# Performance work log

Hardware: AMD Instinct MI355X
Metric: run time of the kernel (lower is better)

The kernel has to match this reference:

```python
import jax, jax.numpy as jnp
import numpy as np

N, D = 8192, 128

def _rbf_kernel(x, y):
    # InfoVAE-style kernel: exp(-mean((x_i - y_j)^2) / dim) = exp(-sqdist / dim^2)
    dim = x.shape[1]
    x2 = jnp.sum(x * x, axis=1)              # [n]
    y2 = jnp.sum(y * y, axis=1)              # [m]
    sqdist = x2[:, None] + y2[None, :] - 2.0 * (x @ y.T)  # [n, m]
    return jnp.exp(-sqdist / (dim * dim))


def setup_inputs() -> dict:
    key = jax.random.key(0)
    k1, k2 = jax.random.split(key)
    inputs = jax.random.normal(k1, (N, D), dtype=jnp.float32)
    true_samples = jax.random.normal(k2, (N, D), dtype=jnp.float32)
    return {"inputs": inputs, "true_samples": true_samples}


def reference(inputs, true_samples):
    x = true_samples  # samples from standard normal prior
    y = inputs
    k_xx = _rbf_kernel(x, x)
    k_yy = _rbf_kernel(y, y)
    k_xy = _rbf_kernel(x, y)
    mmd = jnp.mean(k_xx) + jnp.mean(k_yy) - 2.0 * jnp.mean(k_xy)
    return mmd
```

## Files before the change

kernel.cpp:

```cpp
#include <hip/hip_runtime.h>
#include <hip/hip_bf16.h>
#include <math.h>


#define NN 8192
#define DD 128
#define TZ 16384
#define SPLIT 12
#define NBLK (64 * SPLIT)

typedef __attribute__((ext_vector_type(8))) short bf16x8;
typedef __attribute__((ext_vector_type(4))) float f32x4;
typedef __attribute__((ext_vector_type(2))) float f32x2;

#if __has_builtin(__builtin_amdgcn_exp2f)
#define EXP2F __builtin_amdgcn_exp2f
#else
#define EXP2F exp2f
#endif

constexpr float LOG2E = 0x1.715476p+0f;
constexpr float S2 = LOG2E / 8192.0f;

constexpr size_t PLANE = 1048576;

#define LDS_RED 32768

constexpr size_t WS_NORM = 2048;
constexpr size_t WS_Z    = WS_NORM + (size_t)TZ * sizeof(float);

__device__ __forceinline__ void gload_lds16(const void* g, void* l) {
  __builtin_amdgcn_global_load_lds(
      (const __attribute__((address_space(1))) void*)g,
      (__attribute__((address_space(3))) void*)l, 16, 0, 0);
}

__global__ __launch_bounds__(256) void prep(
    const float* __restrict__ X, const float* __restrict__ Y,
    char* __restrict__ Zs, float* __restrict__ normZ,
    double* __restrict__ sums) {
  if (blockIdx.x == 0) sums[threadIdx.x] = 0.0;

  const int row = blockIdx.x * 4 + (threadIdx.x >> 6);
  const int lane = threadIdx.x & 63;
  const float* __restrict__ src =
      (row < NN) ? (X + (size_t)row * DD) : (Y + (size_t)(row - NN) * DD);
  const float2 v = *reinterpret_cast<const float2*>(src + 2 * lane);

  float n = v.x * v.x + v.y * v.y;

  const int ks = lane >> 4;
  const int quadc = (lane >> 2) & 3;
  const int inner = (lane & 3) * 4;
  char* dst = Zs + (size_t)ks * PLANE + (size_t)row * 64 +
              ((quadc ^ ((row >> 1) & 3)) << 4) + inner;
  *reinterpret_cast<__hip_bfloat162*>(dst) =
      __hip_bfloat162{__float2bfloat16(v.x), __float2bfloat16(v.y)};

#pragma unroll
  for (int o = 32; o > 0; o >>= 1) n += __shfl_down(n, o);
  if (lane == 0) normZ[row] = n * (-LOG2E / 16384.0f);
}

__global__ __launch_bounds__(256, 3) void mmd_mfma(
    const char* __restrict__ Zs, const float* __restrict__ normZ,
    double* __restrict__ sums) {
  __shared__ alignas(16) char lds[LDS_RED + 64];

  const int bid = blockIdx.x;
  const int p = bid / SPLIT, s = bid % SPLIT;
  const int q = 127 - p;
  const int n1 = (127 - p - s) / SPLIT + 1;
  const int u0 = s + SPLIT * n1 - (128 - p);
  const int n2 = (u0 <= p) ? (p - u0) / SPLIT + 1 : 0;

  const int segI[2]  = {p, q};
  const int segJ0[2] = {p + s, q + u0};
  const int segN[2]  = {n1, n2};

  const int tid = threadIdx.x;
  const int lane = tid & 63, wave = tid >> 6;
  const int wr = wave >> 1, wc = wave & 1;
  const int lr = lane & 15, quad = lane >> 4;

  const int csw = (quad ^ ((lr >> 1) & 3)) << 4;
  const char* aRd = lds + (wr * 64 + lr) * 64 + csw;
  const size_t bOff = (size_t)(wc * 64 + lr) * 64 + csw;

  bf16x8 a[4], b0[4], b1[4];
  f32x4 ar[4];

#define LOADA(ks) do {                                                      \
    _Pragma("unroll")                                                       \
    for (int i = 0; i < 4; ++i)                                             \
      a[i] = *reinterpret_cast<const bf16x8*>(aRd + (ks) * 8192 + i * 1024);\
  } while (0)

#define LOADB(dst, base, pl) do {                                           \
    _Pragma("unroll")                                                       \
    for (int j = 0; j < 4; ++j)                                             \
      dst[j] = *reinterpret_cast<const bf16x8*>(                            \
          (base) + (size_t)(pl) * PLANE + j * 1024);                        \
  } while (0)

#define MFMAS(bb) do {                                                      \
    __builtin_amdgcn_s_setprio(1);                                          \
    _Pragma("unroll")                                                       \
    for (int i = 0; i < 4; ++i)                                             \
      _Pragma("unroll")                                                     \
      for (int j = 0; j < 4; ++j)                                           \
        acc[i][j] = __builtin_amdgcn_mfma_f32_16x16x32_bf16(                \
            a[i], bb[j], acc[i][j], 0, 0, 0);                               \
    __builtin_amdgcn_s_setprio(0);                                          \
  } while (0)

  const f32x2 s2v = {S2, S2};
  double blockAcc = 0.0;

  for (int seg = 0; seg < 2; ++seg) {
    const int I = segI[seg];
    const int nIter = segN[seg];
    if (nIter == 0) continue;
    int J = segJ0[seg];

    const float* nzA = normZ + I * 128 + wr * 64;
#pragma unroll
    for (int i = 0; i < 4; ++i)
      ar[i] = *reinterpret_cast<const f32x4*>(nzA + i * 16 + quad * 4);

    const char* srcA0 = Zs + (size_t)(I * 128 + wave * 32) * 64 + lane * 16;
    char* ldwA = lds + wave * 2048;
#pragma unroll
    for (int ks = 0; ks < 4; ++ks) {
      gload_lds16(srcA0 + (size_t)ks * PLANE,        ldwA + ks * 8192);
      gload_lds16(srcA0 + (size_t)ks * PLANE + 1024, ldwA + ks * 8192 + 1024);
    }

    const char* bbase = Zs + (size_t)J * 8192 + bOff;
    LOADB(b0, bbase, 0);
    asm volatile("s_waitcnt vmcnt(0)\n\ts_barrier" ::: "memory");

    for (int it = 0; it < nIter; ++it) {
      const char* bnext = (it + 1 < nIter) ? bbase + SPLIT * 8192 : bbase;
      f32x4 acc[4][4] = {};

      LOADB(b1, bbase, 1);
      LOADA(0);
      __builtin_amdgcn_sched_barrier(0);
      MFMAS(b0);

      LOADB(b0, bbase, 2);
      LOADA(1);
      __builtin_amdgcn_sched_barrier(0);
      MFMAS(b1);

      LOADB(b1, bbase, 3);
      LOADA(2);
      __builtin_amdgcn_sched_barrier(0);
      MFMAS(b0);

      LOADB(b0, bnext, 0);
      LOADA(3);
      __builtin_amdgcn_sched_barrier(0);
      MFMAS(b1);

      const float* nzB = normZ + J * 128 + wc * 64;
      float cb[4];
#pragma unroll
      for (int j = 0; j < 4; ++j) cb[j] = nzB[j * 16 + lr];

      f32x2 part01 = {0.f, 0.f}, part23 = {0.f, 0.f};
#pragma unroll
      for (int i = 0; i < 4; ++i) {
        const f32x2 ar01 = {ar[i].x, ar[i].y};
        const f32x2 ar23 = {ar[i].z, ar[i].w};
#pragma unroll
        for (int j = 0; j < 4; ++j) {
          const f32x2 rb2 = {cb[j], cb[j]};
          const f32x2 base01 = ar01 + rb2;
          const f32x2 base23 = ar23 + rb2;
          const f32x2 acc01 = {acc[i][j][0], acc[i][j][1]};
          const f32x2 acc23 = {acc[i][j][2], acc[i][j][3]};
          const f32x2 arg01 = __builtin_elementwise_fma(acc01, s2v, base01);
          const f32x2 arg23 = __builtin_elementwise_fma(acc23, s2v, base23);
          part01 += (f32x2){EXP2F(arg01.x), EXP2F(arg01.y)};
          part23 += (f32x2){EXP2F(arg23.x), EXP2F(arg23.y)};
        }
      }
      const f32x2 ps = part01 + part23;
      double w = ((I < 64) == (J < 64)) ? 1.0 : -1.0;
      if (I != J) w += w;
      blockAcc += (double)(ps.x + ps.y) * w;

      J += SPLIT;
      bbase = bnext;
    }

    __syncthreads();
  }

#undef LOADA
#undef LOADB
#undef MFMAS

#pragma unroll
  for (int o = 32; o > 0; o >>= 1) blockAcc += __shfl_down(blockAcc, o);
  double* red = reinterpret_cast<double*>(lds + LDS_RED);
  if (lane == 0) red[wave] = blockAcc;
  __syncthreads();
  if (tid == 0)
    atomicAdd(&sums[bid & 255], red[0] + red[1] + red[2] + red[3]);
}

__global__ void finish(const double* __restrict__ s, float* __restrict__ out) {
  double v = s[threadIdx.x] + s[threadIdx.x + 64] + s[threadIdx.x + 128] +
             s[threadIdx.x + 192];
#pragma unroll
  for (int o = 32; o > 0; o >>= 1) v += __shfl_down(v, o);
  if (threadIdx.x == 0)
    out[0] = (float)(v * (1.0 / ((double)NN * (double)NN)));
}

extern "C" void kernel_launch(void* const* d_in, const int* in_sizes, int n_in,
                              void* d_out, int out_size, void* d_ws, size_t ws_size,
                              hipStream_t stream) {
  const float* y_inputs = (const float*)d_in[0];
  const float* x_true   = (const float*)d_in[1];
  float* out = (float*)d_out;

  char* ws = (char*)d_ws;
  double* sums = (double*)ws;
  float* normZ = (float*)(ws + WS_NORM);
  char* Zs = ws + WS_Z;

  prep<<<TZ / 4, 256, 0, stream>>>(x_true, y_inputs, Zs, normZ, sums);
  mmd_mfma<<<NBLK, 256, 0, stream>>>(Zs, normZ, sums);
  finish<<<1, 64, 0, stream>>>(sums, out);
}
```

Before: 101.9 us.

## Keep A tile in registers, halve B tile width, fuse final reduction

Stops staging the A tile in LDS and instead loads all four k-planes of A straight into registers for each segment. B tiles become 64 columns wide, so each block walks twice as many column tiles, and the triangular schedule indexing and sign/weight logic are updated to match. The separate finish kernel is replaced by a last-block-done counter with an atomic-read reduction, which removes one launch. This raises register pressure (16 bf16x8 A fragments) and lowers MFMA work per B load. The setprio hints are also dropped.

```diff
diff --git a/kernel.cpp b/kernel.cpp
--- a/kernel.cpp
+++ b/kernel.cpp
@@ -24,22 +24,18 @@
 
 constexpr size_t PLANE = 1048576;
 
-#define LDS_RED 32768
-
-constexpr size_t WS_NORM = 2048;
+constexpr size_t WS_CTR  = 2048;
+constexpr size_t WS_NORM = 2560;
 constexpr size_t WS_Z    = WS_NORM + (size_t)TZ * sizeof(float);
-
-__device__ __forceinline__ void gload_lds16(const void* g, void* l) {
-  __builtin_amdgcn_global_load_lds(
-      (const __attribute__((address_space(1))) void*)g,
-      (__attribute__((address_space(3))) void*)l, 16, 0, 0);
-}
 
 __global__ __launch_bounds__(256) void prep(
     const float* __restrict__ X, const float* __restrict__ Y,
     char* __restrict__ Zs, float* __restrict__ normZ,
-    double* __restrict__ sums) {
-  if (blockIdx.x == 0) sums[threadIdx.x] = 0.0;
+    double* __restrict__ sums, unsigned* __restrict__ ctr) {
+  if (blockIdx.x == 0) {
+    sums[threadIdx.x] = 0.0;
+    if (threadIdx.x == 0) *ctr = 0u;
+  }
 
   const int row = blockIdx.x * 4 + (threadIdx.x >> 6);
   const int lane = threadIdx.x & 63;
@@ -64,18 +60,17 @@
 
 __global__ __launch_bounds__(256, 3) void mmd_mfma(
     const char* __restrict__ Zs, const float* __restrict__ normZ,
-    double* __restrict__ sums) {
-  __shared__ alignas(16) char lds[LDS_RED + 64];
-
+    double* __restrict__ sums, unsigned* __restrict__ ctr,
+    float* __restrict__ out) {
   const int bid = blockIdx.x;
   const int p = bid / SPLIT, s = bid % SPLIT;
   const int q = 127 - p;
-  const int n1 = (127 - p - s) / SPLIT + 1;
-  const int u0 = s + SPLIT * n1 - (128 - p);
-  const int n2 = (u0 <= p) ? (p - u0) / SPLIT + 1 : 0;
+  const int n1 = (255 - 2 * p - s) / SPLIT + 1;
+  const int u0 = s + SPLIT * n1 - (256 - 2 * p);
+  const int n2 = (u0 <= 2 * p + 1) ? (2 * p + 1 - u0) / SPLIT + 1 : 0;
 
   const int segI[2]  = {p, q};
-  const int segJ0[2] = {p + s, q + u0};
+  const int segJ0[2] = {2 * p + s, 2 * q + u0};
   const int segN[2]  = {n1, n2};
 
   const int tid = threadIdx.x;
@@ -84,34 +79,31 @@
   const int lr = lane & 15, quad = lane >> 4;
 
   const int csw = (quad ^ ((lr >> 1) & 3)) << 4;
-  const char* aRd = lds + (wr * 64 + lr) * 64 + csw;
-  const size_t bOff = (size_t)(wc * 64 + lr) * 64 + csw;
-
-  bf16x8 a[4], b0[4], b1[4];
+
+  bf16x8 aAll[4][4];
+  bf16x8 bA[4], bB[4];
   f32x4 ar[4];
 
-#define LOADA(ks) do {                                                      \
-    _Pragma("unroll")                                                       \
-    for (int i = 0; i < 4; ++i)                                             \
-      a[i] = *reinterpret_cast<const bf16x8*>(aRd + (ks) * 8192 + i * 1024);\
+#define LOADBH(dst, base, pl0) do {                                         \
+    dst[0] = *reinterpret_cast<const bf16x8*>((base) + (size_t)(pl0) * PLANE);        \
+    dst[1] = *reinterpret_cast<const bf16x8*>((base) + (size_t)(pl0) * PLANE + 1024); \
+    dst[2] = *reinterpret_cast<const bf16x8*>((base) + (size_t)(pl0 + 1) * PLANE);    \
+    dst[3] = *reinterpret_cast<const bf16x8*>((base) + (size_t)(pl0 + 1) * PLANE + 1024); \
   } while (0)
 
-#define LOADB(dst, base, pl) do {                                           \
-    _Pragma("unroll")                                                       \
-    for (int j = 0; j < 4; ++j)                                             \
-      dst[j] = *reinterpret_cast<const bf16x8*>(                            \
-          (base) + (size_t)(pl) * PLANE + j * 1024);                        \
-  } while (0)
-
-#define MFMAS(bb) do {                                                      \
-    __builtin_amdgcn_s_setprio(1);                                          \
+#define MFMAH(ks0, bb) do {                                                 \
     _Pragma("unroll")                                                       \
     for (int i = 0; i < 4; ++i)                                             \
       _Pragma("unroll")                                                     \
-      for (int j = 0; j < 4; ++j)                                           \
+      for (int j = 0; j < 2; ++j)                                           \
         acc[i][j] = __builtin_amdgcn_mfma_f32_16x16x32_bf16(                \
-            a[i], bb[j], acc[i][j], 0, 0, 0);                               \
-    __builtin_amdgcn_s_setprio(0);                                          \
+            aAll[ks0][i], bb[j], acc[i][j], 0, 0, 0);                       \
+    _Pragma("unroll")                                                       \
+    for (int i = 0; i < 4; ++i)                                             \
+      _Pragma("unroll")                                                     \
+      for (int j = 0; j < 2; ++j)                                           \
+        acc[i][j] = __builtin_amdgcn_mfma_f32_16x16x32_bf16(                \
+            aAll[ks0 + 1][i], bb[2 + j], acc[i][j], 0, 0, 0);               \
   } while (0)
 
   const f32x2 s2v = {S2, S2};
@@ -128,46 +120,31 @@
     for (int i = 0; i < 4; ++i)
       ar[i] = *reinterpret_cast<const f32x4*>(nzA + i * 16 + quad * 4);
 
-    const char* srcA0 = Zs + (size_t)(I * 128 + wave * 32) * 64 + lane * 16;
-    char* ldwA = lds + wave * 2048;
-#pragma unroll
-    for (int ks = 0; ks < 4; ++ks) {
-      gload_lds16(srcA0 + (size_t)ks * PLANE,        ldwA + ks * 8192);
-      gload_lds16(srcA0 + (size_t)ks * PLANE + 1024, ldwA + ks * 8192 + 1024);
-    }
-
-    const char* bbase = Zs + (size_t)J * 8192 + bOff;
-    LOADB(b0, bbase, 0);
-    asm volatile("s_waitcnt vmcnt(0)\n\ts_barrier" ::: "memory");
+    const char* aBase = Zs + (size_t)(I * 128 + wr * 64 + lr) * 64 + csw;
+#pragma unroll
+    for (int ks = 0; ks < 4; ++ks)
+#pragma unroll
+      for (int i = 0; i < 4; ++i)
+        aAll[ks][i] = *reinterpret_cast<const bf16x8*>(
+            aBase + (size_t)ks * PLANE + i * 1024);
+
+    const char* bbase = Zs + (size_t)(J * 64 + wc * 32 + lr) * 64 + csw;
+    LOADBH(bA, bbase, 0);
 
     for (int it = 0; it < nIter; ++it) {
-      const char* bnext = (it + 1 < nIter) ? bbase + SPLIT * 8192 : bbase;
-      f32x4 acc[4][4] = {};
-
-      LOADB(b1, bbase, 1);
-      LOADA(0);
+      const char* bnext = (it + 1 < nIter) ? bbase + SPLIT * 4096 : bbase;
+      f32x4 acc[4][2] = {};
+
+      LOADBH(bB, bbase, 2);
       __builtin_amdgcn_sched_barrier(0);
-      MFMAS(b0);
-
-      LOADB(b0, bbase, 2);
-      LOADA(1);
+      MFMAH(0, bA);
       __builtin_amdgcn_sched_barrier(0);
-      MFMAS(b1);
-
-      LOADB(b1, bbase, 3);
-      LOADA(2);
+      LOADBH(bA, bnext, 0);
       __builtin_amdgcn_sched_barrier(0);
-      MFMAS(b0);
-
-      LOADB(b0, bnext, 0);
-      LOADA(3);
-      __builtin_amdgcn_sched_barrier(0);
-      MFMAS(b1);
-
-      const float* nzB = normZ + J * 128 + wc * 64;
-      float cb[4];
-#pragma unroll
-      for (int j = 0; j < 4; ++j) cb[j] = nzB[j * 16 + lr];
+      MFMAH(2, bB);
+
+      const float* nzB = normZ + J * 64 + wc * 32;
+      const float cb0 = nzB[lr], cb1 = nzB[16 + lr];
 
       f32x2 part01 = {0.f, 0.f}, part23 = {0.f, 0.f};
 #pragma unroll
@@ -175,8 +152,9 @@
         const f32x2 ar01 = {ar[i].x, ar[i].y};
         const f32x2 ar23 = {ar[i].z, ar[i].w};
 #pragma unroll
-        for (int j = 0; j < 4; ++j) {
-          const f32x2 rb2 = {cb[j], cb[j]};
+        for (int j = 0; j < 2; ++j) {
+          const float rb = j ? cb1 : cb0;
+          const f32x2 rb2 = {rb, rb};
           const f32x2 base01 = ar01 + rb2;
           const f32x2 base23 = ar23 + rb2;
           const f32x2 acc01 = {acc[i][j][0], acc[i][j][1]};
@@ -188,37 +166,40 @@
         }
       }
       const f32x2 ps = part01 + part23;
-      double w = ((I < 64) == (J < 64)) ? 1.0 : -1.0;
-      if (I != J) w += w;
+      double w = ((I < 64) == (J < 128)) ? 1.0 : -1.0;
+      if ((J >> 1) != I) w += w;
       blockAcc += (double)(ps.x + ps.y) * w;
 
       J += SPLIT;
       bbase = bnext;
     }
-
-    __syncthreads();
-  }
-
-#undef LOADA
-#undef LOADB
-#undef MFMAS
-
+  }
+
+#undef LOADBH
+#undef MFMAH
+
+  __shared__ double red[4];
+  __shared__ int lastFlag;
 #pragma unroll
   for (int o = 32; o > 0; o >>= 1) blockAcc += __shfl_down(blockAcc, o);
-  double* red = reinterpret_cast<double*>(lds + LDS_RED);
   if (lane == 0) red[wave] = blockAcc;
   __syncthreads();
-  if (tid == 0)
+  if (tid == 0) {
     atomicAdd(&sums[bid & 255], red[0] + red[1] + red[2] + red[3]);
-}
-
-__global__ void finish(const double* __restrict__ s, float* __restrict__ out) {
-  double v = s[threadIdx.x] + s[threadIdx.x + 64] + s[threadIdx.x + 128] +
-             s[threadIdx.x + 192];
-#pragma unroll
-  for (int o = 32; o > 0; o >>= 1) v += __shfl_down(v, o);
-  if (threadIdx.x == 0)
-    out[0] = (float)(v * (1.0 / ((double)NN * (double)NN)));
+    __threadfence();
+    lastFlag = (atomicAdd(ctr, 1u) == NBLK - 1);
+  }
+  __syncthreads();
+  if (wave == 0 && lastFlag) {
+    double v = 0.0;
+#pragma unroll
+    for (int k = 0; k < 4; ++k)
+      v += atomicAdd(&sums[lane * 4 + k], 0.0);
+#pragma unroll
+    for (int o = 32; o > 0; o >>= 1) v += __shfl_down(v, o);
+    if (lane == 0)
+      out[0] = (float)(v * (1.0 / ((double)NN * (double)NN)));
+  }
 }
 
 extern "C" void kernel_launch(void* const* d_in, const int* in_sizes, int n_in,
@@ -230,10 +211,10 @@
 
   char* ws = (char*)d_ws;
   double* sums = (double*)ws;
+  unsigned* ctr = (unsigned*)(ws + WS_CTR);
   float* normZ = (float*)(ws + WS_NORM);
   char* Zs = ws + WS_Z;
 
-  prep<<<TZ / 4, 256, 0, stream>>>(x_true, y_inputs, Zs, normZ, sums);
-  mmd_mfma<<<NBLK, 256, 0, stream>>>(Zs, normZ, sums);
-  finish<<<1, 64, 0, stream>>>(sums, out);
+  prep<<<TZ / 4, 256, 0, stream>>>(x_true, y_inputs, Zs, normZ, sums, ctr);
+  mmd_mfma<<<NBLK, 256, 0, stream>>>(Zs, normZ, sums, ctr, out);
 }
```

New measurement: 110.0 us. +7.9%, slower.
